# Performance work log

Measured on AMD Instinct MI355X. Metric: run time of the kernel, lower is better.

## Reference

```python
import jax, jax.numpy as jnp
import numpy as np

KERNEL = 7  # neighborhood window (7x7)
NUM_HEADS = 4


def _window_idx(L, k):
    # NATTEN edge-clamped window start: each query attends to exactly k neighbors.
    starts = jnp.clip(jnp.arange(L) - k // 2, 0, L - k)  # [L]
    return starts[:, None] + jnp.arange(k)[None, :]       # [L, k]


def setup_inputs() -> dict:
    key = jax.random.key(0)
    k1, k2, k3, k4, k5 = jax.random.split(key, 5)
    B, H, W, D = 8, 64, 64, 128
    return {
        "x": jax.random.normal(k1, (B, H, W, D), dtype=jnp.float32),
        "w_qkv": jax.random.normal(k2, (3 * D, D), dtype=jnp.float32) * 0.02,
        "b_qkv": jax.random.normal(k3, (3 * D,), dtype=jnp.float32) * 0.02,
        "w_proj": jax.random.normal(k4, (D, D), dtype=jnp.float32) * 0.02,
        "b_proj": jax.random.normal(k5, (D,), dtype=jnp.float32) * 0.02,
    }


def reference(x, w_qkv, b_qkv, w_proj, b_proj):
    B, H, W, D = x.shape
    nh, k = NUM_HEADS, KERNEL
    hd = D // nh
    scale = hd ** -0.5

    # QKV projection -> [3, B, nh, H, W, hd]
    qkv = x @ w_qkv.T + b_qkv
    qkv = qkv.reshape(B, H, W, 3, nh, hd).transpose(3, 0, 4, 1, 2, 5)
    q, kk, v = qkv[0], qkv[1], qkv[2]

    idx_h = _window_idx(H, k)  # [H, k]
    idx_w = _window_idx(W, k)  # [W, k]
    IH = idx_h[:, None, :, None]  # [H,1,k,1]
    IW = idx_w[None, :, None, :]  # [1,W,1,k]

    # Gather local K/V neighborhoods: [B, nh, H, W, k, k, hd] -> [B, nh, H, W, k*k, hd]
    kn = kk[:, :, IH, IW, :].reshape(B, nh, H, W, k * k, hd)
    vn = v[:, :, IH, IW, :].reshape(B, nh, H, W, k * k, hd)

    attn = jnp.einsum('bhxyd,bhxynd->bhxyn', q * scale, kn)
    attn = jax.nn.softmax(attn, axis=-1)
    out = jnp.einsum('bhxyn,bhxynd->bhxyd', attn, vn)

    out = out.transpose(0, 2, 3, 1, 4).reshape(B, H, W, D)
    return out @ w_proj.T + b_proj
```

## Files before the change

kernel.cpp:

```cpp
#include <hip/hip_runtime.h>
#include <hip/hip_bf16.h>

#define BB 8
#define HH 64
#define WW 64
#define DD 128
#define NH 4
#define HD 32
#define KS 7
#define TS 8
#define HALO 14

typedef __attribute__((ext_vector_type(8))) short short8v;
typedef __attribute__((ext_vector_type(4))) short short4v;
typedef __attribute__((ext_vector_type(4))) float f32x4;
typedef unsigned short bf16_t;

__device__ inline bf16_t f2bf(float f) {
  __hip_bfloat16 h = __float2bfloat16(f);
  return *reinterpret_cast<bf16_t*>(&h);
}

__global__ __launch_bounds__(256) void qkv_mfma(
    const float* __restrict__ x, const float* __restrict__ w,
    const float* __restrict__ bqkv,
    bf16_t* __restrict__ q, bf16_t* __restrict__ k, bf16_t* __restrict__ v) {
  __shared__ __align__(16) short smA[64 * 128];
  __shared__ __align__(16) short smB[128 * 128];
  const int tid = threadIdx.x;
  const int m_tile = blockIdx.x;
  const int n_tile = blockIdx.y;

  const float* Ab = x + (size_t)m_tile * 64 * 128;
  const float* Bb = w + (size_t)n_tile * 128 * 128;
#pragma unroll
  for (int i = 0; i < 4; i++) {
    int idx = tid + i * 256;
    int r = idx >> 4, p = idx & 15;
    const float* ap = Ab + r * 128 + p * 8;
    float4 a0 = *(const float4*)ap;
    float4 a1 = *(const float4*)(ap + 4);
    short8v s;
    s[0] = f2bf(a0.x); s[1] = f2bf(a0.y); s[2] = f2bf(a0.z); s[3] = f2bf(a0.w);
    s[4] = f2bf(a1.x); s[5] = f2bf(a1.y); s[6] = f2bf(a1.z); s[7] = f2bf(a1.w);
    *(short8v*)((char*)smA + ((r * 256 + p * 16) ^ ((r & 7) << 4))) = s;
  }
#pragma unroll
  for (int i = 0; i < 8; i++) {
    int idx = tid + i * 256;
    int r = idx >> 4, p = idx & 15;
    const float* bp_ = Bb + r * 128 + p * 8;
    float4 b0 = *(const float4*)bp_;
    float4 b1 = *(const float4*)(bp_ + 4);
    short8v t;
    t[0] = f2bf(b0.x); t[1] = f2bf(b0.y); t[2] = f2bf(b0.z); t[3] = f2bf(b0.w);
    t[4] = f2bf(b1.x); t[5] = f2bf(b1.y); t[6] = f2bf(b1.z); t[7] = f2bf(b1.w);
    *(short8v*)((char*)smB + ((r * 256 + p * 16) ^ ((r & 7) << 4))) = t;
  }
  __syncthreads();

  const int lane = tid & 63, wid = tid >> 6;
  const int wm = wid >> 1, wn = wid & 1;
  const int l15 = lane & 15, l4 = lane >> 4;

  f32x4 acc[2][4] = {};
  const int rowA0 = wm * 32 + l15;
  const int rowB0 = wn * 64 + l15;
  const int swzA = (rowA0 & 7) << 4;
  const int swzB = (rowB0 & 7) << 4;

#pragma unroll
  for (int ks = 0; ks < 4; ks++) {
    const int cb = ks * 64 + l4 * 16;
    short8v a[2], b[4];
#pragma unroll
    for (int mi = 0; mi < 2; mi++)
      a[mi] = *(const short8v*)((const char*)smA +
                ((((rowA0 + mi * 16) * 256) + cb) ^ swzA));
#pragma unroll
    for (int nj = 0; nj < 4; nj++)
      b[nj] = *(const short8v*)((const char*)smB +
                ((((rowB0 + nj * 16) * 256) + cb) ^ swzB));
#pragma unroll
    for (int mi = 0; mi < 2; mi++)
#pragma unroll
      for (int nj = 0; nj < 4; nj++)
        acc[mi][nj] = __builtin_amdgcn_mfma_f32_16x16x32_bf16(a[mi], b[nj], acc[mi][nj], 0, 0, 0);
  }

  __syncthreads();
  short* smC = smA;
  const float qscale = 0.17677669529663687f;
  const float sc = (n_tile == 0) ? qscale : 1.f;
#pragma unroll
  for (int nj = 0; nj < 4; nj++) {
    const int n_local = wn * 64 + nj * 16 + l15;
    const float bias = bqkv[n_tile * 128 + n_local];
#pragma unroll
    for (int mi = 0; mi < 2; mi++) {
#pragma unroll
      for (int r = 0; r < 4; r++) {
        const int m = wm * 32 + mi * 16 + l4 * 4 + r;
        *(bf16_t*)((char*)smC + ((m * 256 + n_local * 2) ^ ((m & 7) << 4))) =
            f2bf((acc[mi][nj][r] + bias) * sc);
      }
    }
  }
  __syncthreads();

  const int bblk = m_tile >> 6;
  bf16_t* outp = (n_tile == 0) ? q : ((n_tile == 1) ? k : v);
#pragma unroll
  for (int i = 0; i < 4; i++) {
    const int idx = i * 256 + tid;
    const int h = idx >> 8;
    const int rem = idx & 255;
    const int m = rem >> 2, c = rem & 3;
    short8v t8 = *(const short8v*)((const char*)smC +
        ((m * 256 + h * 64 + c * 16) ^ ((m & 7) << 4)));
    const int pix = (m_tile * 64 + m) & 4095;
    *(short8v*)(outp + ((size_t)(bblk * 4 + h)) * 131072 + (size_t)pix * 32 + c * 8) = t8;
  }
}

__global__ __launch_bounds__(256) void attn_proj_fused(
    const bf16_t* __restrict__ q, const bf16_t* __restrict__ k,
    const bf16_t* __restrict__ v, const float* __restrict__ wp,
    const float* __restrict__ bpj, float* __restrict__ out) {
  __shared__ __align__(16) char lds[49152];
  char* vtb = lds;
  short* wpb = (short*)(lds + 16384);

  const int tile = blockIdx.x;
  const int tx = tile >> 3, ty = tile & 7;
  const int bb = blockIdx.y;
  const int rstart = min(max(tx * TS - 3, 0), HH - HALO);
  const int cstart = min(max(ty * TS - 3, 0), WW - HALO);
  const int tid = threadIdx.x;
  const int lane = tid & 63, wid = tid >> 6;
  const int l15 = lane & 15, h4 = lane >> 4;
  const size_t bb4 = (size_t)bb * 4;

#pragma unroll
  for (int i = 0; i < 8; i++) {
    int idx = tid + i * 256;
    int r = idx >> 4, p = idx & 15;
    const float* bp_ = wp + r * 128 + p * 8;
    float4 b0 = *(const float4*)bp_;
    float4 b1 = *(const float4*)(bp_ + 4);
    short8v t;
    t[0] = f2bf(b0.x); t[1] = f2bf(b0.y); t[2] = f2bf(b0.z); t[3] = f2bf(b0.w);
    t[4] = f2bf(b1.x); t[5] = f2bf(b1.y); t[6] = f2bf(b1.z); t[7] = f2bf(b1.w);
    *(short8v*)((char*)wpb + ((r * 256 + p * 16) ^ ((r & 7) << 4))) = t;
  }

  int qx, qy;
  {
    const int pit = wid * 16 + l15;
    qx = tx * TS + (pit >> 3);
    qy = ty * TS + (pit & 7);
  }
  const size_t qoff = (size_t)(qx * WW + qy) * HD + h4 * 8;
  const int wx0 = min(max(qx - 3, 0), HH - KS) - rstart;
  const int wy0 = min(max(qy - 3, 0), WW - KS) - cstart;
  const int x0 = tx * TS + wid * 2;
  const int w0 = min(max(x0 - 3, 0), HH - KS) - rstart;
  const int base = min(w0 & ~1, 4);
  bool cv[4];
#pragma unroll
  for (int r = 0; r < 4; r++) cv[r] = ((unsigned)(h4 * 4 + r - wy0) < 7u);
  const int kcol = cstart + min(l15, 13);
  const f32x4 zf = {0.f, 0.f, 0.f, 0.f};

  short8v qf[4];
#pragma unroll
  for (int h = 0; h < 4; h++)
    qf[h] = *(const short8v*)(q + (bb4 + h) * 131072 + qoff);

  short4v vlb[2][4][2];
  {
    const bf16_t* vb0 = v + bb4 * 131072;
#pragma unroll
    for (int t = 0; t < 4; t++) {
      const int idx = tid + t * 256;
      if (idx < 784) {
        const int pp = idx >> 3, c = idx & 7;
        const int pr = pp / 7, pc2 = (pp % 7) * 2;
        const size_t g = ((size_t)((rstart + pr) * WW + (cstart + pc2))) * HD + c * 4;
        vlb[0][t][0] = *(const short4v*)(vb0 + g);
        vlb[0][t][1] = *(const short4v*)(vb0 + g + HD);
      }
    }
  }

  unsigned oph[4][4];

#pragma unroll
  for (int h = 0; h < 4; h++) {
    const bf16_t* kb = k + (bb4 + h) * 131072;

    f32x4 acc[10];
#pragma unroll
    for (int ch = 0; ch < 2; ch++) {
      short8v kf[5];
#pragma unroll
      for (int i = 0; i < 5; i++) {
        const int pr = rstart + base + ch * 5 + i;
        kf[i] = *(const short8v*)(kb + ((size_t)(pr * WW + kcol)) * HD + h4 * 8);
      }
      __builtin_amdgcn_s_setprio(1);
#pragma unroll
      for (int i = 0; i < 5; i++)
        acc[ch * 5 + i] = __builtin_amdgcn_mfma_f32_16x16x32_bf16(kf[i], qf[h], zf, 0, 0, 0);
      __builtin_amdgcn_s_setprio(0);
    }

    if (h > 0) {
      __builtin_amdgcn_sched_barrier(0);
      __builtin_amdgcn_s_barrier();
      __builtin_amdgcn_sched_barrier(0);
    }

#pragma unroll
    for (int t = 0; t < 4; t++) {
      const int idx = tid + t * 256;
      if (idx < 784) {
        const int pp = idx >> 3, c = idx & 7;
        const int pr = pp / 7, pc2 = (pp % 7) * 2;
        const int pos0 = ((pr >> 1) << 5) + ((pc2 >> 2) << 3) + ((pr & 1) << 2) + (pc2 & 3);
#pragma unroll
        for (int j = 0; j < 4; j++) {
          const int d = c * 4 + j;
          const unsigned pk2 = (unsigned)(unsigned short)vlb[h & 1][t][0][j] |
                               ((unsigned)(unsigned short)vlb[h & 1][t][1][j] << 16);
          *(unsigned*)(vtb + ((d * 512 + pos0 * 2) ^ ((d & 7) << 4))) = pk2;
        }
      }
    }
    if (h == 0) {
      for (int idx = tid; idx < 512; idx += 256) {
        const int d = idx >> 4, pr = idx & 15;
        if (pr < 14) {
          const int pos = ((pr >> 1) << 5) + 24 + ((pr & 1) << 2) + 2;
          *(unsigned*)(vtb + ((d * 512 + pos * 2) ^ ((d & 7) << 4))) = 0u;
        }
      }
    }

    if (h < 3) {
      const bf16_t* vbn = v + (bb4 + h + 1) * 131072;
#pragma unroll
      for (int t = 0; t < 4; t++) {
        const int idx = tid + t * 256;
        if (idx < 784) {
          const int pp = idx >> 3, c = idx & 7;
          const int pr = pp / 7, pc2 = (pp % 7) * 2;
          const size_t g = ((size_t)((rstart + pr) * WW + (cstart + pc2))) * HD + c * 4;
          vlb[(h + 1) & 1][t][0] = *(const short4v*)(vbn + g);
          vlb[(h + 1) & 1][t][1] = *(const short4v*)(vbn + g + HD);
        }
      }
    }

    float sum = 0.f;
#pragma unroll
    for (int nt = 0; nt < 10; nt++) {
      const bool rv = ((unsigned)(base + nt - wx0) < 7u);
#pragma unroll
      for (int r = 0; r < 4; r++) {
        const float p = (rv && cv[r]) ? __expf(acc[nt][r]) : 0.f;
        acc[nt][r] = p;
        sum += p;
      }
    }
    sum += __shfl_xor(sum, 16);
    sum += __shfl_xor(sum, 32);
    const float inv = 1.f / sum;

    asm volatile("s_waitcnt lgkmcnt(0)" ::: "memory");
    __builtin_amdgcn_sched_barrier(0);
    __builtin_amdgcn_s_barrier();
    __builtin_amdgcn_sched_barrier(0);

    f32x4 o0 = zf, o1 = zf;
    const int swzv = (l15 & 7) << 4;
    const int cbase = (base >> 1) * 64;
    __builtin_amdgcn_s_setprio(1);
#pragma unroll
    for (int kc = 0; kc < 5; kc++) {
      union { unsigned u[4]; short8v s; } pa;
      pa.u[0] = (unsigned)f2bf(acc[2 * kc][0] * inv) |
                ((unsigned)f2bf(acc[2 * kc][1] * inv) << 16);
      pa.u[1] = (unsigned)f2bf(acc[2 * kc][2] * inv) |
                ((unsigned)f2bf(acc[2 * kc][3] * inv) << 16);
      pa.u[2] = (unsigned)f2bf(acc[2 * kc + 1][0] * inv) |
                ((unsigned)f2bf(acc[2 * kc + 1][1] * inv) << 16);
      pa.u[3] = (unsigned)f2bf(acc[2 * kc + 1][2] * inv) |
                ((unsigned)f2bf(acc[2 * kc + 1][3] * inv) << 16);
      const int boff = cbase + kc * 64 + h4 * 16;
      short8v vb0 = *(const short8v*)(vtb + ((l15 * 512 + boff) ^ swzv));
      short8v vb1 = *(const short8v*)(vtb + (((l15 + 16) * 512 + boff) ^ swzv));
      o0 = __builtin_amdgcn_mfma_f32_16x16x32_bf16(pa.s, vb0, o0, 0, 0, 0);
      o1 = __builtin_amdgcn_mfma_f32_16x16x32_bf16(pa.s, vb1, o1, 0, 0, 0);
    }
    __builtin_amdgcn_s_setprio(0);

    oph[h][0] = (unsigned)f2bf(o0[0]) | ((unsigned)f2bf(o0[1]) << 16);
    oph[h][1] = (unsigned)f2bf(o0[2]) | ((unsigned)f2bf(o0[3]) << 16);
    oph[h][2] = (unsigned)f2bf(o1[0]) | ((unsigned)f2bf(o1[1]) << 16);
    oph[h][3] = (unsigned)f2bf(o1[2]) | ((unsigned)f2bf(o1[3]) << 16);
  }
  __syncthreads();

#pragma unroll
  for (int h = 0; h < 4; h++) {
#pragma unroll
    for (int j = 0; j < 4; j++) {
      const unsigned u = oph[h][j];
      const int row0 = wid * 16 + h4 * 4 + (j & 1) * 2;
      const int d = h * 32 + (j >> 1) * 16 + l15;
      *(bf16_t*)(vtb + ((row0 * 256 + d * 2) ^ ((row0 & 7) << 4))) = (bf16_t)(u & 0xFFFFu);
      const int row1 = row0 + 1;
      *(bf16_t*)(vtb + ((row1 * 256 + d * 2) ^ ((row1 & 7) << 4))) = (bf16_t)(u >> 16);
    }
  }
  __syncthreads();

  const int wm = wid >> 1, wn = wid & 1;
  const int l4 = lane >> 4;
  f32x4 pacc[2][4] = {};
  const int rowA0 = wm * 32 + l15;
  const int rowB0 = wn * 64 + l15;
  const int swzA = (rowA0 & 7) << 4;
  const int swzB = (rowB0 & 7) << 4;

#pragma unroll
  for (int ks = 0; ks < 4; ks++) {
    const int cb = ks * 64 + l4 * 16;
    short8v a[2], b[4];
#pragma unroll
    for (int mi = 0; mi < 2; mi++)
      a[mi] = *(const short8v*)(vtb + ((((rowA0 + mi * 16) * 256) + cb) ^ swzA));
#pragma unroll
    for (int nj = 0; nj < 4; nj++)
      b[nj] = *(const short8v*)((const char*)wpb +
                ((((rowB0 + nj * 16) * 256) + cb) ^ swzB));
    __builtin_amdgcn_s_setprio(1);
#pragma unroll
    for (int mi = 0; mi < 2; mi++)
#pragma unroll
      for (int nj = 0; nj < 4; nj++)
        pacc[mi][nj] = __builtin_amdgcn_mfma_f32_16x16x32_bf16(a[mi], b[nj], pacc[mi][nj], 0, 0, 0);
    __builtin_amdgcn_s_setprio(0);
  }

  __syncthreads();
  char* smC = lds + 16384;
#pragma unroll
  for (int nj = 0; nj < 4; nj++) {
    const int n = wn * 64 + nj * 16 + l15;
    const float bias = bpj[n];
#pragma unroll
    for (int mi = 0; mi < 2; mi++) {
#pragma unroll
      for (int r = 0; r < 4; r++) {
        const int m = wm * 32 + mi * 16 + l4 * 4 + r;
        *(float*)(smC + ((m * 512 + n * 4) ^ ((m & 7) << 5))) = pacc[mi][nj][r] + bias;
      }
    }
  }
  __syncthreads();

  float* obase = out + ((size_t)bb * 4096 + (size_t)(tx * TS) * WW + ty * TS) * DD;
#pragma unroll
  for (int i = 0; i < 8; i++) {
    const int idx = i * 256 + tid;
    const int m = idx >> 5, c = idx & 31;
    float4 t = *(const float4*)(smC + ((m * 512 + c * 16) ^ ((m & 7) << 5)));
    const size_t grow = (size_t)(m >> 3) * WW + (m & 7);
    *(float4*)(obase + grow * DD + c * 4) = t;
  }
}

extern "C" void kernel_launch(void* const* d_in, const int* in_sizes, int n_in,
                              void* d_out, int out_size, void* d_ws, size_t ws_size,
                              hipStream_t stream) {
  const float* x      = (const float*)d_in[0];
  const float* w_qkv  = (const float*)d_in[1];
  const float* b_qkv  = (const float*)d_in[2];
  const float* w_proj = (const float*)d_in[3];
  const float* b_proj = (const float*)d_in[4];
  float* out = (float*)d_out;

  const size_t per = (size_t)BB * NH * HH * WW * HD;
  bf16_t* q = (bf16_t*)d_ws;
  bf16_t* k = q + per;
  bf16_t* v = k + per;

  qkv_mfma<<<dim3(512, 3), dim3(256), 0, stream>>>(x, w_qkv, b_qkv, q, k, v);
  attn_proj_fused<<<dim3(64, BB), dim3(256), 0, stream>>>(q, k, v, w_proj, b_proj, out);
}
```

Measured before the change: 40.48 us.

## Process attention heads in pairs with double-size LDS V staging

The per-head loop becomes a loop over head pairs. The two heads' V tiles are staged side by side in LDS (which grows from 48KB to 64KB), so each pair needs one round of block barriers instead of two, and both heads' QK MFMAs are issued back to back. The goal is to cut barrier count and add instruction-level parallelism in the score/softmax stage. In exchange, register use roughly doubles for accumulators and V prefetch, and the larger LDS can lower occupancy.

Measured after the change: 48.68 us. +20.3%, slower.

```diff
diff --git a/kernel.cpp b/kernel.cpp
--- a/kernel.cpp
+++ b/kernel.cpp
@@ -127,9 +127,9 @@
     const bf16_t* __restrict__ q, const bf16_t* __restrict__ k,
     const bf16_t* __restrict__ v, const float* __restrict__ wp,
     const float* __restrict__ bpj, float* __restrict__ out) {
-  __shared__ __align__(16) char lds[49152];
+  __shared__ __align__(16) char lds[65536];
   char* vtb = lds;
-  short* wpb = (short*)(lds + 16384);
+  short* wpb = (short*)(lds + 32768);
 
   const int tile = blockIdx.x;
   const int tx = tile >> 3, ty = tile & 7;
@@ -177,9 +177,10 @@
   for (int h = 0; h < 4; h++)
     qf[h] = *(const short8v*)(q + (bb4 + h) * 131072 + qoff);
 
-  short4v vlb[2][4][2];
-  {
-    const bf16_t* vb0 = v + bb4 * 131072;
+  short4v vl[2][4][2];
+#pragma unroll
+  for (int h = 0; h < 2; h++) {
+    const bf16_t* vb0 = v + (bb4 + h) * 131072;
 #pragma unroll
     for (int t = 0; t < 4; t++) {
       const int idx = tid + t * 256;
@@ -187,8 +188,8 @@
         const int pp = idx >> 3, c = idx & 7;
         const int pr = pp / 7, pc2 = (pp % 7) * 2;
         const size_t g = ((size_t)((rstart + pr) * WW + (cstart + pc2))) * HD + c * 4;
-        vlb[0][t][0] = *(const short4v*)(vb0 + g);
-        vlb[0][t][1] = *(const short4v*)(vb0 + g + HD);
+        vl[h][t][0] = *(const short4v*)(vb0 + g);
+        vl[h][t][1] = *(const short4v*)(vb0 + g + HD);
       }
     }
   }
@@ -196,119 +197,155 @@
   unsigned oph[4][4];
 
 #pragma unroll
-  for (int h = 0; h < 4; h++) {
-    const bf16_t* kb = k + (bb4 + h) * 131072;
-
-    f32x4 acc[10];
-#pragma unroll
-    for (int ch = 0; ch < 2; ch++) {
-      short8v kf[5];
-#pragma unroll
-      for (int i = 0; i < 5; i++) {
-        const int pr = rstart + base + ch * 5 + i;
-        kf[i] = *(const short8v*)(kb + ((size_t)(pr * WW + kcol)) * HD + h4 * 8);
-      }
-      __builtin_amdgcn_s_setprio(1);
-#pragma unroll
-      for (int i = 0; i < 5; i++)
-        acc[ch * 5 + i] = __builtin_amdgcn_mfma_f32_16x16x32_bf16(kf[i], qf[h], zf, 0, 0, 0);
-      __builtin_amdgcn_s_setprio(0);
-    }
-
-    if (h > 0) {
+  for (int hp = 0; hp < 2; hp++) {
+    f32x4 accA[10], accB[10];
+#pragma unroll
+    for (int hh = 0; hh < 2; hh++) {
+      const bf16_t* kb = k + (bb4 + hp * 2 + hh) * 131072;
+      f32x4* accp = hh ? accB : accA;
+      const short8v qfh = qf[hp * 2 + hh];
+#pragma unroll
+      for (int ch = 0; ch < 2; ch++) {
+        short8v kf[5];
+#pragma unroll
+        for (int i = 0; i < 5; i++) {
+          const int pr = rstart + base + ch * 5 + i;
+          kf[i] = *(const short8v*)(kb + ((size_t)(pr * WW + kcol)) * HD + h4 * 8);
+        }
+        __builtin_amdgcn_s_setprio(1);
+#pragma unroll
+        for (int i = 0; i < 5; i++)
+          accp[ch * 5 + i] = __builtin_amdgcn_mfma_f32_16x16x32_bf16(kf[i], qfh, zf, 0, 0, 0);
+        __builtin_amdgcn_s_setprio(0);
+      }
+    }
+
+    if (hp > 0) {
       __builtin_amdgcn_sched_barrier(0);
       __builtin_amdgcn_s_barrier();
       __builtin_amdgcn_sched_barrier(0);
     }
 
 #pragma unroll
-    for (int t = 0; t < 4; t++) {
-      const int idx = tid + t * 256;
-      if (idx < 784) {
-        const int pp = idx >> 3, c = idx & 7;
-        const int pr = pp / 7, pc2 = (pp % 7) * 2;
-        const int pos0 = ((pr >> 1) << 5) + ((pc2 >> 2) << 3) + ((pr & 1) << 2) + (pc2 & 3);
-#pragma unroll
-        for (int j = 0; j < 4; j++) {
-          const int d = c * 4 + j;
-          const unsigned pk2 = (unsigned)(unsigned short)vlb[h & 1][t][0][j] |
-                               ((unsigned)(unsigned short)vlb[h & 1][t][1][j] << 16);
-          *(unsigned*)(vtb + ((d * 512 + pos0 * 2) ^ ((d & 7) << 4))) = pk2;
-        }
-      }
-    }
-    if (h == 0) {
-      for (int idx = tid; idx < 512; idx += 256) {
-        const int d = idx >> 4, pr = idx & 15;
-        if (pr < 14) {
-          const int pos = ((pr >> 1) << 5) + 24 + ((pr & 1) << 2) + 2;
-          *(unsigned*)(vtb + ((d * 512 + pos * 2) ^ ((d & 7) << 4))) = 0u;
-        }
-      }
-    }
-
-    if (h < 3) {
-      const bf16_t* vbn = v + (bb4 + h + 1) * 131072;
+    for (int hh = 0; hh < 2; hh++) {
+      char* vth = vtb + hh * 16384;
 #pragma unroll
       for (int t = 0; t < 4; t++) {
         const int idx = tid + t * 256;
         if (idx < 784) {
           const int pp = idx >> 3, c = idx & 7;
           const int pr = pp / 7, pc2 = (pp % 7) * 2;
-          const size_t g = ((size_t)((rstart + pr) * WW + (cstart + pc2))) * HD + c * 4;
-          vlb[(h + 1) & 1][t][0] = *(const short4v*)(vbn + g);
-          vlb[(h + 1) & 1][t][1] = *(const short4v*)(vbn + g + HD);
-        }
-      }
-    }
-
-    float sum = 0.f;
-#pragma unroll
-    for (int nt = 0; nt < 10; nt++) {
-      const bool rv = ((unsigned)(base + nt - wx0) < 7u);
-#pragma unroll
-      for (int r = 0; r < 4; r++) {
-        const float p = (rv && cv[r]) ? __expf(acc[nt][r]) : 0.f;
-        acc[nt][r] = p;
-        sum += p;
-      }
-    }
-    sum += __shfl_xor(sum, 16);
-    sum += __shfl_xor(sum, 32);
-    const float inv = 1.f / sum;
+          const int pos0 = ((pr >> 1) << 5) + ((pc2 >> 2) << 3) + ((pr & 1) << 2) + (pc2 & 3);
+#pragma unroll
+          for (int j = 0; j < 4; j++) {
+            const int d = c * 4 + j;
+            const unsigned pk2 = (unsigned)(unsigned short)vl[hh][t][0][j] |
+                                 ((unsigned)(unsigned short)vl[hh][t][1][j] << 16);
+            *(unsigned*)(vth + ((d * 512 + pos0 * 2) ^ ((d & 7) << 4))) = pk2;
+          }
+        }
+      }
+    }
+    if (hp == 0) {
+      for (int idx = tid; idx < 1024; idx += 256) {
+        const int half = idx >> 9;
+        const int r2 = idx & 511;
+        const int d = r2 >> 4, pr = r2 & 15;
+        if (pr < 14) {
+          const int pos = ((pr >> 1) << 5) + 24 + ((pr & 1) << 2) + 2;
+          *(unsigned*)(vtb + half * 16384 + ((d * 512 + pos * 2) ^ ((d & 7) << 4))) = 0u;
+        }
+      }
+#pragma unroll
+      for (int h = 0; h < 2; h++) {
+        const bf16_t* vbn = v + (bb4 + 2 + h) * 131072;
+#pragma unroll
+        for (int t = 0; t < 4; t++) {
+          const int idx = tid + t * 256;
+          if (idx < 784) {
+            const int pp = idx >> 3, c = idx & 7;
+            const int pr = pp / 7, pc2 = (pp % 7) * 2;
+            const size_t g = ((size_t)((rstart + pr) * WW + (cstart + pc2))) * HD + c * 4;
+            vl[h][t][0] = *(const short4v*)(vbn + g);
+            vl[h][t][1] = *(const short4v*)(vbn + g + HD);
+          }
+        }
+      }
+    }
+
+    float invA, invB;
+    {
+      float sum = 0.f;
+#pragma unroll
+      for (int nt = 0; nt < 10; nt++) {
+        const bool rv = ((unsigned)(base + nt - wx0) < 7u);
+#pragma unroll
+        for (int r = 0; r < 4; r++) {
+          const float p = (rv && cv[r]) ? __expf(accA[nt][r]) : 0.f;
+          accA[nt][r] = p;
+          sum += p;
+        }
+      }
+      sum += __shfl_xor(sum, 16);
+      sum += __shfl_xor(sum, 32);
+      invA = 1.f / sum;
+    }
+    {
+      float sum = 0.f;
+#pragma unroll
+      for (int nt = 0; nt < 10; nt++) {
+        const bool rv = ((unsigned)(base + nt - wx0) < 7u);
+#pragma unroll
+        for (int r = 0; r < 4; r++) {
+          const float p = (rv && cv[r]) ? __expf(accB[nt][r]) : 0.f;
+          accB[nt][r] = p;
+          sum += p;
+        }
+      }
+      sum += __shfl_xor(sum, 16);
+      sum += __shfl_xor(sum, 32);
+      invB = 1.f / sum;
+    }
 
     asm volatile("s_waitcnt lgkmcnt(0)" ::: "memory");
     __builtin_amdgcn_sched_barrier(0);
     __builtin_amdgcn_s_barrier();
     __builtin_amdgcn_sched_barrier(0);
 
-    f32x4 o0 = zf, o1 = zf;
     const int swzv = (l15 & 7) << 4;
     const int cbase = (base >> 1) * 64;
-    __builtin_amdgcn_s_setprio(1);
-#pragma unroll
-    for (int kc = 0; kc < 5; kc++) {
-      union { unsigned u[4]; short8v s; } pa;
-      pa.u[0] = (unsigned)f2bf(acc[2 * kc][0] * inv) |
-                ((unsigned)f2bf(acc[2 * kc][1] * inv) << 16);
-      pa.u[1] = (unsigned)f2bf(acc[2 * kc][2] * inv) |
-                ((unsigned)f2bf(acc[2 * kc][3] * inv) << 16);
-      pa.u[2] = (unsigned)f2bf(acc[2 * kc + 1][0] * inv) |
-                ((unsigned)f2bf(acc[2 * kc + 1][1] * inv) << 16);
-      pa.u[3] = (unsigned)f2bf(acc[2 * kc + 1][2] * inv) |
-                ((unsigned)f2bf(acc[2 * kc + 1][3] * inv) << 16);
-      const int boff = cbase + kc * 64 + h4 * 16;
-      short8v vb0 = *(const short8v*)(vtb + ((l15 * 512 + boff) ^ swzv));
-      short8v vb1 = *(const short8v*)(vtb + (((l15 + 16) * 512 + boff) ^ swzv));
-      o0 = __builtin_amdgcn_mfma_f32_16x16x32_bf16(pa.s, vb0, o0, 0, 0, 0);
-      o1 = __builtin_amdgcn_mfma_f32_16x16x32_bf16(pa.s, vb1, o1, 0, 0, 0);
-    }
-    __builtin_amdgcn_s_setprio(0);
-
-    oph[h][0] = (unsigned)f2bf(o0[0]) | ((unsigned)f2bf(o0[1]) << 16);
-    oph[h][1] = (unsigned)f2bf(o0[2]) | ((unsigned)f2bf(o0[3]) << 16);
-    oph[h][2] = (unsigned)f2bf(o1[0]) | ((unsigned)f2bf(o1[1]) << 16);
-    oph[h][3] = (unsigned)f2bf(o1[2]) | ((unsigned)f2bf(o1[3]) << 16);
+#pragma unroll
+    for (int hh = 0; hh < 2; hh++) {
+      const f32x4* accp = hh ? accB : accA;
+      const float inv = hh ? invB : invA;
+      char* vth = vtb + hh * 16384;
+      f32x4 o0 = zf, o1 = zf;
+      __builtin_amdgcn_s_setprio(1);
+#pragma unroll
+      for (int kc = 0; kc < 5; kc++) {
+        union { unsigned u[4]; short8v s; } pa;
+        pa.u[0] = (unsigned)f2bf(accp[2 * kc][0] * inv) |
+                  ((unsigned)f2bf(accp[2 * kc][1] * inv) << 16);
+        pa.u[1] = (unsigned)f2bf(accp[2 * kc][2] * inv) |
+                  ((unsigned)f2bf(accp[2 * kc][3] * inv) << 16);
+        pa.u[2] = (unsigned)f2bf(accp[2 * kc + 1][0] * inv) |
+                  ((unsigned)f2bf(accp[2 * kc + 1][1] * inv) << 16);
+        pa.u[3] = (unsigned)f2bf(accp[2 * kc + 1][2] * inv) |
+                  ((unsigned)f2bf(accp[2 * kc + 1][3] * inv) << 16);
+        const int boff = cbase + kc * 64 + h4 * 16;
+        short8v vb0 = *(const short8v*)(vth + ((l15 * 512 + boff) ^ swzv));
+        short8v vb1 = *(const short8v*)(vth + (((l15 + 16) * 512 + boff) ^ swzv));
+        o0 = __builtin_amdgcn_mfma_f32_16x16x32_bf16(pa.s, vb0, o0, 0, 0, 0);
+        o1 = __builtin_amdgcn_mfma_f32_16x16x32_bf16(pa.s, vb1, o1, 0, 0, 0);
+      }
+      __builtin_amdgcn_s_setprio(0);
+
+      const int h = hp * 2 + hh;
+      oph[h][0] = (unsigned)f2bf(o0[0]) | ((unsigned)f2bf(o0[1]) << 16);
+      oph[h][1] = (unsigned)f2bf(o0[2]) | ((unsigned)f2bf(o0[3]) << 16);
+      oph[h][2] = (unsigned)f2bf(o1[0]) | ((unsigned)f2bf(o1[1]) << 16);
+      oph[h][3] = (unsigned)f2bf(o1[2]) | ((unsigned)f2bf(o1[3]) << 16);
+    }
   }
   __syncthreads();
 
@@ -355,7 +392,7 @@
   }
 
   __syncthreads();
-  char* smC = lds + 16384;
+  char* smC = lds + 32768;
 #pragma unroll
   for (int nj = 0; nj < 4; nj++) {
     const int n = wn * 64 + nj * 16 + l15;
```

## Double block size to 512 threads, split heads across wave halves

Applied to the files above, without the earlier changes.

Both kernels now launch with 512 threads per block instead of 256. In the QKV GEMM each wave computes a 32x32 output tile rather than 32x64. In the fused attention kernel the two wave halves each take one head of every head pair, so two heads run at once with separate V-transpose LDS buffers. LDS grows to 64KB, and the V prefetch changes from a double-buffered register array to a single prefetch of the second head pair. This aims to put more waves on each CU for the small 512-block attention grid and halve the serial per-head loop, at the cost of more LDS and possibly lower blocks-per-CU occupancy.

After: 41.90 us. 3.5% more time.

```diff
diff --git a/kernel.cpp b/kernel.cpp
--- a/kernel.cpp
+++ b/kernel.cpp
@@ -21,7 +21,7 @@
   return *reinterpret_cast<bf16_t*>(&h);
 }
 
-__global__ __launch_bounds__(256) void qkv_mfma(
+__global__ __launch_bounds__(512) void qkv_mfma(
     const float* __restrict__ x, const float* __restrict__ w,
     const float* __restrict__ bqkv,
     bf16_t* __restrict__ q, bf16_t* __restrict__ k, bf16_t* __restrict__ v) {
@@ -34,8 +34,8 @@
   const float* Ab = x + (size_t)m_tile * 64 * 128;
   const float* Bb = w + (size_t)n_tile * 128 * 128;
 #pragma unroll
-  for (int i = 0; i < 4; i++) {
-    int idx = tid + i * 256;
+  for (int i = 0; i < 2; i++) {
+    int idx = tid + i * 512;
     int r = idx >> 4, p = idx & 15;
     const float* ap = Ab + r * 128 + p * 8;
     float4 a0 = *(const float4*)ap;
@@ -46,8 +46,8 @@
     *(short8v*)((char*)smA + ((r * 256 + p * 16) ^ ((r & 7) << 4))) = s;
   }
 #pragma unroll
-  for (int i = 0; i < 8; i++) {
-    int idx = tid + i * 256;
+  for (int i = 0; i < 4; i++) {
+    int idx = tid + i * 512;
     int r = idx >> 4, p = idx & 15;
     const float* bp_ = Bb + r * 128 + p * 8;
     float4 b0 = *(const float4*)bp_;
@@ -60,31 +60,31 @@
   __syncthreads();
 
   const int lane = tid & 63, wid = tid >> 6;
-  const int wm = wid >> 1, wn = wid & 1;
+  const int wm = wid >> 2, wn = wid & 3;
   const int l15 = lane & 15, l4 = lane >> 4;
 
-  f32x4 acc[2][4] = {};
+  f32x4 acc[2][2] = {};
   const int rowA0 = wm * 32 + l15;
-  const int rowB0 = wn * 64 + l15;
+  const int rowB0 = wn * 32 + l15;
   const int swzA = (rowA0 & 7) << 4;
   const int swzB = (rowB0 & 7) << 4;
 
 #pragma unroll
   for (int ks = 0; ks < 4; ks++) {
     const int cb = ks * 64 + l4 * 16;
-    short8v a[2], b[4];
+    short8v a[2], b[2];
 #pragma unroll
     for (int mi = 0; mi < 2; mi++)
       a[mi] = *(const short8v*)((const char*)smA +
                 ((((rowA0 + mi * 16) * 256) + cb) ^ swzA));
 #pragma unroll
-    for (int nj = 0; nj < 4; nj++)
+    for (int nj = 0; nj < 2; nj++)
       b[nj] = *(const short8v*)((const char*)smB +
                 ((((rowB0 + nj * 16) * 256) + cb) ^ swzB));
 #pragma unroll
     for (int mi = 0; mi < 2; mi++)
 #pragma unroll
-      for (int nj = 0; nj < 4; nj++)
+      for (int nj = 0; nj < 2; nj++)
         acc[mi][nj] = __builtin_amdgcn_mfma_f32_16x16x32_bf16(a[mi], b[nj], acc[mi][nj], 0, 0, 0);
   }
 
@@ -93,8 +93,8 @@
   const float qscale = 0.17677669529663687f;
   const float sc = (n_tile == 0) ? qscale : 1.f;
 #pragma unroll
-  for (int nj = 0; nj < 4; nj++) {
-    const int n_local = wn * 64 + nj * 16 + l15;
+  for (int nj = 0; nj < 2; nj++) {
+    const int n_local = wn * 32 + nj * 16 + l15;
     const float bias = bqkv[n_tile * 128 + n_local];
 #pragma unroll
     for (int mi = 0; mi < 2; mi++) {
@@ -111,8 +111,8 @@
   const int bblk = m_tile >> 6;
   bf16_t* outp = (n_tile == 0) ? q : ((n_tile == 1) ? k : v);
 #pragma unroll
-  for (int i = 0; i < 4; i++) {
-    const int idx = i * 256 + tid;
+  for (int i = 0; i < 2; i++) {
+    const int idx = i * 512 + tid;
     const int h = idx >> 8;
     const int rem = idx & 255;
     const int m = rem >> 2, c = rem & 3;
@@ -123,13 +123,13 @@
   }
 }
 
-__global__ __launch_bounds__(256) void attn_proj_fused(
+__global__ __launch_bounds__(512) void attn_proj_fused(
     const bf16_t* __restrict__ q, const bf16_t* __restrict__ k,
     const bf16_t* __restrict__ v, const float* __restrict__ wp,
     const float* __restrict__ bpj, float* __restrict__ out) {
-  __shared__ __align__(16) char lds[49152];
+  __shared__ __align__(16) char lds[65536];
   char* vtb = lds;
-  short* wpb = (short*)(lds + 16384);
+  short* wpb = (short*)(lds + 32768);
 
   const int tile = blockIdx.x;
   const int tx = tile >> 3, ty = tile & 7;
@@ -138,12 +138,16 @@
   const int cstart = min(max(ty * TS - 3, 0), WW - HALO);
   const int tid = threadIdx.x;
   const int lane = tid & 63, wid = tid >> 6;
+  const int g = wid & 3;
+  const int wh = wid >> 2;
+  const int hh = tid >> 8;
+  const int tid2 = tid & 255;
   const int l15 = lane & 15, h4 = lane >> 4;
   const size_t bb4 = (size_t)bb * 4;
 
 #pragma unroll
-  for (int i = 0; i < 8; i++) {
-    int idx = tid + i * 256;
+  for (int i = 0; i < 4; i++) {
+    int idx = tid + i * 512;
     int r = idx >> 4, p = idx & 15;
     const float* bp_ = wp + r * 128 + p * 8;
     float4 b0 = *(const float4*)bp_;
@@ -156,14 +160,14 @@
 
   int qx, qy;
   {
-    const int pit = wid * 16 + l15;
+    const int pit = g * 16 + l15;
     qx = tx * TS + (pit >> 3);
     qy = ty * TS + (pit & 7);
   }
   const size_t qoff = (size_t)(qx * WW + qy) * HD + h4 * 8;
   const int wx0 = min(max(qx - 3, 0), HH - KS) - rstart;
   const int wy0 = min(max(qy - 3, 0), WW - KS) - cstart;
-  const int x0 = tx * TS + wid * 2;
+  const int x0 = tx * TS + g * 2;
   const int w0 = min(max(x0 - 3, 0), HH - KS) - rstart;
   const int base = min(w0 & ~1, 4);
   bool cv[4];
@@ -172,32 +176,34 @@
   const int kcol = cstart + min(l15, 13);
   const f32x4 zf = {0.f, 0.f, 0.f, 0.f};
 
-  short8v qf[4];
-#pragma unroll
-  for (int h = 0; h < 4; h++)
-    qf[h] = *(const short8v*)(q + (bb4 + h) * 131072 + qoff);
-
-  short4v vlb[2][4][2];
+  short8v qf[2];
+#pragma unroll
+  for (int hp = 0; hp < 2; hp++)
+    qf[hp] = *(const short8v*)(q + (bb4 + hp * 2 + wh) * 131072 + qoff);
+
+  short4v vl[4][2];
   {
-    const bf16_t* vb0 = v + bb4 * 131072;
+    const bf16_t* vb0 = v + (bb4 + hh) * 131072;
 #pragma unroll
     for (int t = 0; t < 4; t++) {
-      const int idx = tid + t * 256;
+      const int idx = tid2 + t * 256;
       if (idx < 784) {
         const int pp = idx >> 3, c = idx & 7;
         const int pr = pp / 7, pc2 = (pp % 7) * 2;
-        const size_t g = ((size_t)((rstart + pr) * WW + (cstart + pc2))) * HD + c * 4;
-        vlb[0][t][0] = *(const short4v*)(vb0 + g);
-        vlb[0][t][1] = *(const short4v*)(vb0 + g + HD);
-      }
-    }
-  }
-
-  unsigned oph[4][4];
-
-#pragma unroll
-  for (int h = 0; h < 4; h++) {
-    const bf16_t* kb = k + (bb4 + h) * 131072;
+        const size_t g2 = ((size_t)((rstart + pr) * WW + (cstart + pc2))) * HD + c * 4;
+        vl[t][0] = *(const short4v*)(vb0 + g2);
+        vl[t][1] = *(const short4v*)(vb0 + g2 + HD);
+      }
+    }
+  }
+
+  unsigned oph[2][4];
+  char* vth = vtb + wh * 16384;
+  char* vtw = vtb + hh * 16384;
+
+#pragma unroll
+  for (int hp = 0; hp < 2; hp++) {
+    const bf16_t* kb = k + (bb4 + hp * 2 + wh) * 131072;
 
     f32x4 acc[10];
 #pragma unroll
@@ -211,11 +217,11 @@
       __builtin_amdgcn_s_setprio(1);
 #pragma unroll
       for (int i = 0; i < 5; i++)
-        acc[ch * 5 + i] = __builtin_amdgcn_mfma_f32_16x16x32_bf16(kf[i], qf[h], zf, 0, 0, 0);
+        acc[ch * 5 + i] = __builtin_amdgcn_mfma_f32_16x16x32_bf16(kf[i], qf[hp], zf, 0, 0, 0);
       __builtin_amdgcn_s_setprio(0);
     }
 
-    if (h > 0) {
+    if (hp > 0) {
       __builtin_amdgcn_sched_barrier(0);
       __builtin_amdgcn_s_barrier();
       __builtin_amdgcn_sched_barrier(0);
@@ -223,7 +229,7 @@
 
 #pragma unroll
     for (int t = 0; t < 4; t++) {
-      const int idx = tid + t * 256;
+      const int idx = tid2 + t * 256;
       if (idx < 784) {
         const int pp = idx >> 3, c = idx & 7;
         const int pr = pp / 7, pc2 = (pp % 7) * 2;
@@ -231,33 +237,32 @@
 #pragma unroll
         for (int j = 0; j < 4; j++) {
           const int d = c * 4 + j;
-          const unsigned pk2 = (unsigned)(unsigned short)vlb[h & 1][t][0][j] |
-                               ((unsigned)(unsigned short)vlb[h & 1][t][1][j] << 16);
-          *(unsigned*)(vtb + ((d * 512 + pos0 * 2) ^ ((d & 7) << 4))) = pk2;
+          const unsigned pk2 = (unsigned)(unsigned short)vl[t][0][j] |
+                               ((unsigned)(unsigned short)vl[t][1][j] << 16);
+          *(unsigned*)(vtw + ((d * 512 + pos0 * 2) ^ ((d & 7) << 4))) = pk2;
         }
       }
     }
-    if (h == 0) {
-      for (int idx = tid; idx < 512; idx += 256) {
+    if (hp == 0) {
+#pragma unroll
+      for (int t = 0; t < 2; t++) {
+        const int idx = tid2 + t * 256;
         const int d = idx >> 4, pr = idx & 15;
         if (pr < 14) {
           const int pos = ((pr >> 1) << 5) + 24 + ((pr & 1) << 2) + 2;
-          *(unsigned*)(vtb + ((d * 512 + pos * 2) ^ ((d & 7) << 4))) = 0u;
+          *(unsigned*)(vtw + ((d * 512 + pos * 2) ^ ((d & 7) << 4))) = 0u;
         }
       }
-    }
-
-    if (h < 3) {
-      const bf16_t* vbn = v + (bb4 + h + 1) * 131072;
+      const bf16_t* vbn = v + (bb4 + 2 + hh) * 131072;
 #pragma unroll
       for (int t = 0; t < 4; t++) {
-        const int idx = tid + t * 256;
+        const int idx = tid2 + t * 256;
         if (idx < 784) {
           const int pp = idx >> 3, c = idx & 7;
           const int pr = pp / 7, pc2 = (pp % 7) * 2;
-          const size_t g = ((size_t)((rstart + pr) * WW + (cstart + pc2))) * HD + c * 4;
-          vlb[(h + 1) & 1][t][0] = *(const short4v*)(vbn + g);
-          vlb[(h + 1) & 1][t][1] = *(const short4v*)(vbn + g + HD);
+          const size_t g2 = ((size_t)((rstart + pr) * WW + (cstart + pc2))) * HD + c * 4;
+          vl[t][0] = *(const short4v*)(vbn + g2);
+          vl[t][1] = *(const short4v*)(vbn + g2 + HD);
         }
       }
     }
@@ -298,26 +303,27 @@
       pa.u[3] = (unsigned)f2bf(acc[2 * kc + 1][2] * inv) |
                 ((unsigned)f2bf(acc[2 * kc + 1][3] * inv) << 16);
       const int boff = cbase + kc * 64 + h4 * 16;
-      short8v vb0 = *(const short8v*)(vtb + ((l15 * 512 + boff) ^ swzv));
-      short8v vb1 = *(const short8v*)(vtb + (((l15 + 16) * 512 + boff) ^ swzv));
+      short8v vb0 = *(const short8v*)(vth + ((l15 * 512 + boff) ^ swzv));
+      short8v vb1 = *(const short8v*)(vth + (((l15 + 16) * 512 + boff) ^ swzv));
       o0 = __builtin_amdgcn_mfma_f32_16x16x32_bf16(pa.s, vb0, o0, 0, 0, 0);
       o1 = __builtin_amdgcn_mfma_f32_16x16x32_bf16(pa.s, vb1, o1, 0, 0, 0);
     }
     __builtin_amdgcn_s_setprio(0);
 
-    oph[h][0] = (unsigned)f2bf(o0[0]) | ((unsigned)f2bf(o0[1]) << 16);
-    oph[h][1] = (unsigned)f2bf(o0[2]) | ((unsigned)f2bf(o0[3]) << 16);
-    oph[h][2] = (unsigned)f2bf(o1[0]) | ((unsigned)f2bf(o1[1]) << 16);
-    oph[h][3] = (unsigned)f2bf(o1[2]) | ((unsigned)f2bf(o1[3]) << 16);
-  }
-  __syncthreads();
-
-#pragma unroll
-  for (int h = 0; h < 4; h++) {
+    oph[hp][0] = (unsigned)f2bf(o0[0]) | ((unsigned)f2bf(o0[1]) << 16);
+    oph[hp][1] = (unsigned)f2bf(o0[2]) | ((unsigned)f2bf(o0[3]) << 16);
+    oph[hp][2] = (unsigned)f2bf(o1[0]) | ((unsigned)f2bf(o1[1]) << 16);
+    oph[hp][3] = (unsigned)f2bf(o1[2]) | ((unsigned)f2bf(o1[3]) << 16);
+  }
+  __syncthreads();
+
+#pragma unroll
+  for (int hp = 0; hp < 2; hp++) {
+    const int h = hp * 2 + wh;
 #pragma unroll
     for (int j = 0; j < 4; j++) {
-      const unsigned u = oph[h][j];
-      const int row0 = wid * 16 + h4 * 4 + (j & 1) * 2;
+      const unsigned u = oph[hp][j];
+      const int row0 = g * 16 + h4 * 4 + (j & 1) * 2;
       const int d = h * 32 + (j >> 1) * 16 + l15;
       *(bf16_t*)(vtb + ((row0 * 256 + d * 2) ^ ((row0 & 7) << 4))) = (bf16_t)(u & 0xFFFFu);
       const int row1 = row0 + 1;
@@ -326,39 +332,39 @@
   }
   __syncthreads();
 
-  const int wm = wid >> 1, wn = wid & 1;
+  const int wm = wid >> 2, wn = wid & 3;
   const int l4 = lane >> 4;
-  f32x4 pacc[2][4] = {};
+  f32x4 pacc[2][2] = {};
   const int rowA0 = wm * 32 + l15;
-  const int rowB0 = wn * 64 + l15;
+  const int rowB0 = wn * 32 + l15;
   const int swzA = (rowA0 & 7) << 4;
   const int swzB = (rowB0 & 7) << 4;
 
 #pragma unroll
   for (int ks = 0; ks < 4; ks++) {
     const int cb = ks * 64 + l4 * 16;
-    short8v a[2], b[4];
+    short8v a[2], b[2];
 #pragma unroll
     for (int mi = 0; mi < 2; mi++)
       a[mi] = *(const short8v*)(vtb + ((((rowA0 + mi * 16) * 256) + cb) ^ swzA));
 #pragma unroll
-    for (int nj = 0; nj < 4; nj++)
+    for (int nj = 0; nj < 2; nj++)
       b[nj] = *(const short8v*)((const char*)wpb +
                 ((((rowB0 + nj * 16) * 256) + cb) ^ swzB));
     __builtin_amdgcn_s_setprio(1);
 #pragma unroll
     for (int mi = 0; mi < 2; mi++)
 #pragma unroll
-      for (int nj = 0; nj < 4; nj++)
+      for (int nj = 0; nj < 2; nj++)
         pacc[mi][nj] = __builtin_amdgcn_mfma_f32_16x16x32_bf16(a[mi], b[nj], pacc[mi][nj], 0, 0, 0);
     __builtin_amdgcn_s_setprio(0);
   }
 
   __syncthreads();
-  char* smC = lds + 16384;
-#pragma unroll
-  for (int nj = 0; nj < 4; nj++) {
-    const int n = wn * 64 + nj * 16 + l15;
+  char* smC = lds + 32768;
+#pragma unroll
+  for (int nj = 0; nj < 2; nj++) {
+    const int n = wn * 32 + nj * 16 + l15;
     const float bias = bpj[n];
 #pragma unroll
     for (int mi = 0; mi < 2; mi++) {
@@ -373,8 +379,8 @@
 
   float* obase = out + ((size_t)bb * 4096 + (size_t)(tx * TS) * WW + ty * TS) * DD;
 #pragma unroll
-  for (int i = 0; i < 8; i++) {
-    const int idx = i * 256 + tid;
+  for (int i = 0; i < 4; i++) {
+    const int idx = i * 512 + tid;
     const int m = idx >> 5, c = idx & 31;
     float4 t = *(const float4*)(smC + ((m * 512 + c * 16) ^ ((m & 7) << 5)));
     const size_t grow = (size_t)(m >> 3) * WW + (m & 7);
@@ -397,6 +403,6 @@
   bf16_t* k = q + per;
   bf16_t* v = k + per;
 
-  qkv_mfma<<<dim3(512, 3), dim3(256), 0, stream>>>(x, w_qkv, b_qkv, q, k, v);
-  attn_proj_fused<<<dim3(64, BB), dim3(256), 0, stream>>>(q, k, v, w_proj, b_proj, out);
+  qkv_mfma<<<dim3(512, 3), dim3(512), 0, stream>>>(x, w_qkv, b_qkv, q, k, v);
+  attn_proj_fused<<<dim3(64, BB), dim3(512), 0, stream>>>(q, k, v, w_proj, b_proj, out);
 }
```
